# Optimization experiments

Measured on AMD Instinct MI355X. Metric: run time of the kernel, lower is better.

Reference implementation:

```python
import jax, jax.numpy as jnp
import numpy as np

B, S, D = 2, 2048, 1024
H, E = 16, 64


def setup_inputs() -> dict:
    key = jax.random.key(0)
    k1, k2, k3, k4 = jax.random.split(key, 4)
    x = jax.random.normal(k1, (B, S, D), dtype=jnp.float32)
    # per-head Q/K/V projection weights, stacked over the head axis
    scale = 1.0 / np.sqrt(D)
    Wq = jax.random.normal(k2, (H, D, E), dtype=jnp.float32) * scale
    Wk = jax.random.normal(k3, (H, D, E), dtype=jnp.float32) * scale
    Wv = jax.random.normal(k4, (H, D, E), dtype=jnp.float32) * scale
    return {"x": x, "Wq": Wq, "Wk": Wk, "Wv": Wv}


def reference(x, Wq, Wk, Wv):
    # Grouped-over-heads equivalent of the per-head torch loop.
    q = jnp.einsum("bsd,hde->bhse", x, Wq)  # [B,H,S,E]
    k = jnp.einsum("bsd,hde->bhse", x, Wk)
    v = jnp.einsum("bsd,hde->bhse", x, Wv)

    scores = jnp.einsum("bhse,bhte->bhst", q, k)  # [B,H,S,S]
    scores = scores / jnp.sqrt(jnp.asarray(E, dtype=scores.dtype))
    causal = jnp.tril(jnp.ones((S, S), dtype=bool))  # True on/below diagonal
    scores = jnp.where(causal, scores, jnp.finfo(scores.dtype).min)
    attn = jax.nn.softmax(scores, axis=-1)  # dropout p=0.0 -> identity

    out = jnp.einsum("bhst,bhte->bhse", attn, v)  # [B,H,S,E]
    # concat over heads on the last dim, matching torch.concat(..., dim=-1)
    return out.transpose(0, 2, 1, 3).reshape(B, S, H * E)
```

## Files before the change

### kernel.cpp

```cpp
#include <hip/hip_runtime.h>
#include <stdint.h>

#define S_LEN 2048
#define D_DIM 1024
#define NB 2
#define NH 16
#define NE 64
#define N_COLS (3 * NH * NE)
#define QK_COLS 2048
#define K_DIM D_DIM

typedef unsigned short u16;
typedef unsigned int u32;
typedef unsigned long long u64;
typedef u16 u16x8 __attribute__((ext_vector_type(8)));
typedef __bf16 bf16x8 __attribute__((ext_vector_type(8)));
typedef float f32x4 __attribute__((ext_vector_type(4)));

__device__ __forceinline__ u16 f2b(float f) {
  u32 u = __builtin_bit_cast(u32, f);
  return (u16)((u + 0x7FFFu + ((u >> 16) & 1u)) >> 16);
}

__device__ __forceinline__ void gload_lds16(const void* g, void* l) {
  __builtin_amdgcn_global_load_lds(
      (const __attribute__((address_space(1))) u32*)g,
      (__attribute__((address_space(3))) u32*)l, 16, 0, 0);
}

__global__ __launch_bounds__(256) void k_prep(const float* __restrict__ x,
                                              const float* __restrict__ Wq,
                                              const float* __restrict__ Wk,
                                              const float* __restrict__ Wv,
                                              u16* __restrict__ xb,
                                              u16* __restrict__ Wt) {
  __shared__ u16 tile[64][65];
  int bid = blockIdx.x;
  int t = threadIdx.x;
  if (bid < 2048) {
    size_t i = (size_t)bid * 256 + t;
    const float4* xf = (const float4*)x;
    float4 a = xf[2 * i], c = xf[2 * i + 1];
    u16x8 o;
    o[0] = f2b(a.x); o[1] = f2b(a.y); o[2] = f2b(a.z); o[3] = f2b(a.w);
    o[4] = f2b(c.x); o[5] = f2b(c.y); o[6] = f2b(c.z); o[7] = f2b(c.w);
    *(u16x8*)(xb + 8 * i) = o;
  } else {
    int wbid = bid - 2048;
    int kb = wbid & 15;
    int h = (wbid >> 4) & 15;
    int proj = wbid >> 8;
    const float* W = (proj == 0) ? Wq : ((proj == 1) ? Wk : Wv);
    int k0 = kb * 64;
    int e = t & 63, kr = t >> 6;
    const float* src = W + ((size_t)h * D_DIM + k0 + kr * 16) * NE + e;
#pragma unroll
    for (int j = 0; j < 16; ++j) tile[kr * 16 + j][e] = f2b(src[(size_t)j * NE]);
    __syncthreads();
    int e2 = t >> 2, kc = (t & 3) * 16;
    u16x8 o0, o1;
#pragma unroll
    for (int j = 0; j < 8; ++j) { o0[j] = tile[kc + j][e2]; o1[j] = tile[kc + 8 + j][e2]; }
    size_t n = (size_t)proj * 1024 + h * 64 + e2;
    u16* dst = Wt + n * K_DIM + k0 + kc;
    *(u16x8*)dst = o0;
    *(u16x8*)(dst + 8) = o1;
  }
}

__global__ __launch_bounds__(256) void k_gemm(const u16* __restrict__ A,
                                              const u16* __restrict__ Bt,
                                              u16* __restrict__ Cqk,
                                              u16* __restrict__ VT) {
  __shared__ __align__(16) u16 As[128 * 64];
  __shared__ __align__(16) u16 Bs[128 * 64];
  int t = threadIdx.x;
  int lane = t & 63, w = t >> 6;
  int hi = lane >> 4, l15 = lane & 15;
  int wr = (w >> 1) * 64, wc = (w & 1) * 64;
  int bid = blockIdx.x;
  int xcd = bid & 7, r0 = bid >> 3;
  int m0 = (r0 / 3) * 128;
  int n0 = (xcd * 3 + (r0 % 3)) * 128;
  bool isV = (n0 >= 2048);
  float qscale = ((n0 + wc) < 1024) ? 0.18033688f : 1.0f;
  f32x4 acc[4][4];
#pragma unroll
  for (int m = 0; m < 4; m++)
#pragma unroll
    for (int n = 0; n < 4; n++)
#pragma unroll
      for (int j = 0; j < 4; j++) acc[m][n][j] = 0.f;

  for (int k0 = 0; k0 < K_DIM; k0 += 64) {
#pragma unroll
    for (int i = 0; i < 4; ++i) {
      int ci = i * 256 + t;
      int row = ci >> 3, c = ci & 7;
      int cs = c ^ (row & 7);
      gload_lds16(A + (size_t)(m0 + row) * K_DIM + k0 + cs * 8,
                  (char*)As + (size_t)(i * 256 + w * 64) * 16);
      gload_lds16(Bt + (size_t)(n0 + row) * K_DIM + k0 + cs * 8,
                  (char*)Bs + (size_t)(i * 256 + w * 64) * 16);
    }
    __syncthreads();
#pragma unroll
    for (int ks = 0; ks < 2; ++ks) {
      int kc = ks * 4 + hi;
      bf16x8 af[4], bfr[4];
#pragma unroll
      for (int m = 0; m < 4; m++) {
        int r = wr + m * 16 + l15;
        af[m] = *(const bf16x8*)&As[r * 64 + ((kc ^ (r & 7)) * 8)];
      }
#pragma unroll
      for (int n = 0; n < 4; n++) {
        int r = wc + n * 16 + l15;
        bfr[n] = *(const bf16x8*)&Bs[r * 64 + ((kc ^ (r & 7)) * 8)];
      }
#pragma unroll
      for (int m = 0; m < 4; m++)
#pragma unroll
        for (int n = 0; n < 4; n++)
          acc[m][n] = __builtin_amdgcn_mfma_f32_16x16x32_bf16(af[m], bfr[n], acc[m][n], 0, 0, 0);
    }
    __syncthreads();
  }

  if (!isV) {
#pragma unroll
    for (int m = 0; m < 4; m++) {
#pragma unroll
      for (int r = 0; r < 4; r++) {
        int row = m0 + wr + m * 16 + hi * 4 + r;
#pragma unroll
        for (int n = 0; n < 4; n++) {
          int col = n0 + wc + n * 16 + l15;
          Cqk[(size_t)row * QK_COLS + col] = f2b(acc[m][n][r] * qscale);
        }
      }
    }
  } else {
#pragma unroll
    for (int m = 0; m < 4; m++) {
      int row_s = m0 + wr + m * 16 + hi * 4;
      int bb = row_s >> 11, s = row_s & 2047;
      int pos = (s & ~63) | (s & 32) | ((s & 12) << 1) | ((s & 16) >> 2) | (s & 3);
#pragma unroll
      for (int n = 0; n < 4; n++) {
        int col = n0 + wc + n * 16 + l15 - 2048;
        int hh = col >> 6, e = col & 63;
        u64 pk = (u64)f2b(acc[m][n][0]) | ((u64)f2b(acc[m][n][1]) << 16) |
                 ((u64)f2b(acc[m][n][2]) << 32) | ((u64)f2b(acc[m][n][3]) << 48);
        *(u64*)(VT + ((size_t)((bb * 16 + hh) * 64 + e)) * S_LEN + pos) = pk;
      }
    }
  }
}

__device__ __forceinline__ void stage_k(const u16* kb_, u16* kdst, int kv0, int t, int w) {
#pragma unroll
  for (int i = 0; i < 2; ++i) {
    int ci = i * 256 + t;
    int row = ci >> 3, c = ci & 7;
    int cs = c ^ (row & 7);
    gload_lds16(kb_ + (size_t)(kv0 + row) * QK_COLS + cs * 8,
                (char*)kdst + (size_t)(i * 256 + w * 64) * 16);
  }
}

__device__ __forceinline__ void stage_v(const u16* vtb_, u16* vdst, int kv0, int t, int w) {
#pragma unroll
  for (int i = 0; i < 2; ++i) {
    int ci = i * 256 + t;
    int row = ci >> 3, c = ci & 7;
    int cs = c ^ (row & 7);
    gload_lds16(vtb_ + (size_t)row * S_LEN + kv0 + cs * 8,
                (char*)vdst + (size_t)(i * 256 + w * 64) * 16);
  }
}

__global__ __launch_bounds__(256) void k_attn(const u16* __restrict__ qk,
                                              const u16* __restrict__ VT,
                                              float* __restrict__ out) {
  __shared__ __align__(16) u16 Ks[2][64 * 64];
  __shared__ __align__(16) u16 Vs[2][64 * 64];
  int t = threadIdx.x;
  int lane = t & 63, w = t >> 6;
  int hi = lane >> 4, l15 = lane & 15;
  int bid = blockIdx.x;
  int x = bid & 7, g = bid >> 3;
  int bh = x * 4 + (g & 3);
  int qt = 31 - (g >> 2);
  int b = bh >> 4, h = bh & 15;
  const u16* qb_ = qk + (size_t)b * S_LEN * QK_COLS + h * NE;
  const u16* kb_ = qb_ + 1024;
  const u16* vtb_ = VT + (size_t)bh * 64 * S_LEN;

  int q0 = qt * 64;
  int nt = qt + 1;
  int wqb = q0 + w * 16;

  bf16x8 qf[2];
#pragma unroll
  for (int ks = 0; ks < 2; ks++)
    qf[ks] = *(const bf16x8*)(qb_ + (size_t)(wqb + l15) * QK_COLS + ks * 32 + hi * 8);

  f32x4 o[4];
#pragma unroll
  for (int i = 0; i < 4; i++)
#pragma unroll
    for (int j = 0; j < 4; j++) o[i][j] = 0.f;
  float lsum = 0.f;
  int myq = wqb + l15;

  stage_k(kb_, Ks[0], 0, t, w);
  stage_v(vtb_, Vs[0], 0, t, w);
  __syncthreads();

  int cur = 0;
  for (int ti = 0; ti < nt; ++ti) {
    int kv0 = ti * 64;
    bool pf = (ti + 1 < nt);
    if (pf) {
      stage_k(kb_, Ks[cur ^ 1], kv0 + 64, t, w);
      stage_v(vtb_, Vs[cur ^ 1], kv0 + 64, t, w);
    }

    f32x4 s[4];
#pragma unroll
    for (int f = 0; f < 4; f++)
#pragma unroll
      for (int j = 0; j < 4; j++) s[f][j] = 0.f;
    __builtin_amdgcn_s_setprio(1);
#pragma unroll
    for (int ks = 0; ks < 2; ks++) {
      int kc = ks * 4 + hi;
#pragma unroll
      for (int f = 0; f < 4; f++) {
        int r = f * 16 + l15;
        bf16x8 kf = *(const bf16x8*)&Ks[cur][r * 64 + ((kc ^ (r & 7)) * 8)];
        s[f] = __builtin_amdgcn_mfma_f32_16x16x32_bf16(kf, qf[ks], s[f], 0, 0, 0);
      }
    }
    __builtin_amdgcn_s_setprio(0);

    bool diag = (ti == nt - 1);
#pragma unroll
    for (int f = 0; f < 4; f++) {
#pragma unroll
      for (int r = 0; r < 4; r++) {
        float p = __builtin_amdgcn_exp2f(s[f][r]);
        if (diag) {
          int kv = kv0 + f * 16 + 4 * hi + r;
          p = (kv <= myq) ? p : 0.f;
        }
        s[f][r] = p;
        lsum += p;
      }
    }

    __builtin_amdgcn_s_setprio(1);
#pragma unroll
    for (int ks = 0; ks < 2; ks++) {
      bf16x8 pa;
#pragma unroll
      for (int j = 0; j < 4; j++) {
        pa[j] = (__bf16)s[2 * ks][j];
        pa[4 + j] = (__bf16)s[2 * ks + 1][j];
      }
#pragma unroll
      for (int ef = 0; ef < 4; ef++) {
        int e = ef * 16 + l15;
        bf16x8 vbf = *(const bf16x8*)&Vs[cur][e * 64 + (((4 * ks + hi) ^ (e & 7)) * 8)];
        o[ef] = __builtin_amdgcn_mfma_f32_16x16x32_bf16(pa, vbf, o[ef], 0, 0, 0);
      }
    }
    __builtin_amdgcn_s_setprio(0);
    __syncthreads();
    cur ^= 1;
  }

  lsum += __shfl_xor(lsum, 16);
  lsum += __shfl_xor(lsum, 32);
#pragma unroll
  for (int r = 0; r < 4; r++) {
    float l = __shfl(lsum, 4 * hi + r);
    float inv = 1.0f / l;
    int q = wqb + 4 * hi + r;
#pragma unroll
    for (int ef = 0; ef < 4; ef++) {
      int col = h * NE + ef * 16 + l15;
      out[((size_t)b * S_LEN + q) * (NH * NE) + col] = o[ef][r] * inv;
    }
  }
}

extern "C" void kernel_launch(void* const* d_in, const int* in_sizes, int n_in,
                              void* d_out, int out_size, void* d_ws, size_t ws_size,
                              hipStream_t stream) {
  const float* x = (const float*)d_in[0];
  const float* Wq = (const float*)d_in[1];
  const float* Wk = (const float*)d_in[2];
  const float* Wv = (const float*)d_in[3];
  float* out = (float*)d_out;

  char* ws = (char*)d_ws;
  u16* xb = (u16*)ws;
  u16* Wt = (u16*)(ws + (8u << 20));
  u16* qk = (u16*)(ws + (14u << 20));
  u16* VT = (u16*)(ws + (30u << 20));

  k_prep<<<dim3(2816), dim3(256), 0, stream>>>(x, Wq, Wk, Wv, xb, Wt);
  k_gemm<<<dim3(768), dim3(256), 0, stream>>>(xb, Wt, qk, VT);
  k_attn<<<dim3(1024), dim3(256), 0, stream>>>(qk, VT, out);
}
```

Baseline: 86.29 us.

## Compute V^T directly by swapping GEMM operands and permute K rows instead

The V-projection blocks now compute Wv^T·x^T, so the output tile is already transposed and is stored with row-contiguous 2-byte writes into VT instead of scattered permuted 8-byte stores. The key-position permutation that used to be baked into the VT layout is moved to K staging: K rows are loaded in sigma64 order and the causal mask uses the same permutation. The aim is coalesced V^T stores and a simpler tile-to-block mapping for V, at the cost of narrower stores and extra index arithmetic in attention staging.

```diff
diff --git a/kernel.cpp b/kernel.cpp
--- a/kernel.cpp
+++ b/kernel.cpp
@@ -6,13 +6,11 @@
 #define NB 2
 #define NH 16
 #define NE 64
-#define N_COLS (3 * NH * NE)
 #define QK_COLS 2048
 #define K_DIM D_DIM
 
 typedef unsigned short u16;
 typedef unsigned int u32;
-typedef unsigned long long u64;
 typedef u16 u16x8 __attribute__((ext_vector_type(8)));
 typedef __bf16 bf16x8 __attribute__((ext_vector_type(8)));
 typedef float f32x4 __attribute__((ext_vector_type(4)));
@@ -26,6 +24,10 @@
   __builtin_amdgcn_global_load_lds(
       (const __attribute__((address_space(1))) u32*)g,
       (__attribute__((address_space(3))) u32*)l, 16, 0, 0);
+}
+
+__device__ __forceinline__ int sigma64(int m) {
+  return (m & 32) | ((m & 12) << 1) | ((m & 16) >> 2) | (m & 3);
 }
 
 __global__ __launch_bounds__(256) void k_prep(const float* __restrict__ x,
@@ -80,10 +82,21 @@
   int wr = (w >> 1) * 64, wc = (w & 1) * 64;
   int bid = blockIdx.x;
   int xcd = bid & 7, r0 = bid >> 3;
-  int m0 = (r0 / 3) * 128;
-  int n0 = (xcd * 3 + (r0 % 3)) * 128;
-  bool isV = (n0 >= 2048);
-  float qscale = ((n0 + wc) < 1024) ? 0.18033688f : 1.0f;
+  bool isV = (r0 >= 64);
+  int m0, n0;
+  const u16 *arows, *brows;
+  if (!isV) {
+    m0 = (r0 >> 1) * 128;
+    n0 = (xcd * 2 + (r0 & 1)) * 128;
+    arows = A + (size_t)m0 * K_DIM;
+    brows = Bt + (size_t)n0 * K_DIM;
+  } else {
+    m0 = xcd * 128;
+    n0 = (r0 - 64) * 128;
+    arows = Bt + (size_t)(2048 + m0) * K_DIM;
+    brows = A + (size_t)n0 * K_DIM;
+  }
+  float qscale = (!isV && (n0 + wc) < 1024) ? 0.18033688f : 1.0f;
   f32x4 acc[4][4];
 #pragma unroll
   for (int m = 0; m < 4; m++)
@@ -98,9 +111,9 @@
       int ci = i * 256 + t;
       int row = ci >> 3, c = ci & 7;
       int cs = c ^ (row & 7);
-      gload_lds16(A + (size_t)(m0 + row) * K_DIM + k0 + cs * 8,
+      gload_lds16(arows + (size_t)row * K_DIM + k0 + cs * 8,
                   (char*)As + (size_t)(i * 256 + w * 64) * 16);
-      gload_lds16(Bt + (size_t)(n0 + row) * K_DIM + k0 + cs * 8,
+      gload_lds16(brows + (size_t)row * K_DIM + k0 + cs * 8,
                   (char*)Bs + (size_t)(i * 256 + w * 64) * 16);
     }
     __syncthreads();
@@ -143,16 +156,15 @@
   } else {
 #pragma unroll
     for (int m = 0; m < 4; m++) {
-      int row_s = m0 + wr + m * 16 + hi * 4;
-      int bb = row_s >> 11, s = row_s & 2047;
-      int pos = (s & ~63) | (s & 32) | ((s & 12) << 1) | ((s & 16) >> 2) | (s & 3);
-#pragma unroll
-      for (int n = 0; n < 4; n++) {
-        int col = n0 + wc + n * 16 + l15 - 2048;
-        int hh = col >> 6, e = col & 63;
-        u64 pk = (u64)f2b(acc[m][n][0]) | ((u64)f2b(acc[m][n][1]) << 16) |
-                 ((u64)f2b(acc[m][n][2]) << 32) | ((u64)f2b(acc[m][n][3]) << 48);
-        *(u64*)(VT + ((size_t)((bb * 16 + hh) * 64 + e)) * S_LEN + pos) = pk;
+#pragma unroll
+      for (int r = 0; r < 4; r++) {
+        int vrow = m0 + wr + m * 16 + hi * 4 + r;
+#pragma unroll
+        for (int n = 0; n < 4; n++) {
+          int col = n0 + wc + n * 16 + l15;
+          VT[(size_t)((col >> 11) * 1024 + vrow) * S_LEN + (col & 2047)] =
+              f2b(acc[m][n][r]);
+        }
       }
     }
   }
@@ -163,8 +175,9 @@
   for (int i = 0; i < 2; ++i) {
     int ci = i * 256 + t;
     int row = ci >> 3, c = ci & 7;
+    int srow = sigma64(row);
     int cs = c ^ (row & 7);
-    gload_lds16(kb_ + (size_t)(kv0 + row) * QK_COLS + cs * 8,
+    gload_lds16(kb_ + (size_t)(kv0 + srow) * QK_COLS + cs * 8,
                 (char*)kdst + (size_t)(i * 256 + w * 64) * 16);
   }
 }
@@ -252,7 +265,7 @@
       for (int r = 0; r < 4; r++) {
         float p = __builtin_amdgcn_exp2f(s[f][r]);
         if (diag) {
-          int kv = kv0 + f * 16 + 4 * hi + r;
+          int kv = kv0 + sigma64(16 * f + 4 * hi + r);
           p = (kv <= myq) ? p : 0.f;
         }
         s[f][r] = p;
```

Measured after the change: 88.25 us. +2.3%, slower.
